# Optimization experiments

Hardware: AMD Instinct MI355X
Metric: run time of the kernel (lower is better)

The kernel has to match this reference:

```python
import jax, jax.numpy as jnp
import numpy as np

TAU = 0.9
TOPK = 8
NUM_LAYERS = 3


def _layer_norm(x, g, b, eps=1e-5):
    mu = jnp.mean(x, axis=-1, keepdims=True)
    var = jnp.var(x, axis=-1, keepdims=True)
    return (x - mu) / jnp.sqrt(var + eps) * g + b


def _forward(x, edge_index, Wi, bi, wp, Wa, ba, ln1_g, ln1_b, ln2_g, ln2_b,
             W1, b1, W2, b2, Wc, bc, Wo, bo):
    N = x.shape[0]
    H = Wi.shape[1]
    # input projection + relu
    x = jax.nn.relu(x @ Wi + bi)
    src, dst = edge_index[0], edge_index[1]
    # ---- priority pi (computed under no_grad, dummy_alpha = 1, x_prev = 0) ----
    delta_x = jnp.sum(jnp.abs(x), axis=1)                      # [N]
    neigh = jax.ops.segment_sum(delta_x[src], dst, num_segments=N)
    pi = jax.lax.stop_gradient(jax.nn.sigmoid(x @ wp + neigh))  # [N]
    # ---- add self loops (selected subgraph == full graph) ----
    loops = jnp.arange(N, dtype=src.dtype)
    src_e = jnp.concatenate([src, loops])
    dst_e = jnp.concatenate([dst, loops])
    Et = src_e.shape[0]
    # ---- edge attention logits: att_mlp(cat[h_i, h_j, p_j]) computed as split matvec ----
    a_dst = x @ Wa[:H]          # contribution of h_i = x[dst]
    a_src = x @ Wa[H:2 * H]     # contribution of h_j = x[src]
    e = a_dst[dst_e] + a_src[src_e] + pi[src_e] * Wa[2 * H] + ba[0]
    e = jax.nn.leaky_relu(e, 0.2) / TAU
    e = jnp.clip(e, -5.0, 5.0)
    exp_e = jnp.exp(e)
    denom = jax.ops.segment_sum(exp_e, dst_e, num_segments=N)
    alpha = exp_e / (denom[dst_e] + 1e-16)
    # ---- per-destination top-k sparsification + renormalization (vectorized) ----
    order = jnp.lexsort((-alpha, dst_e))       # sort by dst, then alpha descending
    dst_s = dst_e[order]
    alpha_s = alpha[order]
    pos = jnp.arange(Et)
    is_new = jnp.concatenate([jnp.ones((1,), bool), dst_s[1:] != dst_s[:-1]])
    grp_start = jax.lax.cummax(jnp.where(is_new, pos, 0))
    rank = pos - grp_start                     # rank within each dst group
    keep = rank < TOPK
    ksum = jax.ops.segment_sum(jnp.where(keep, alpha_s, 0.0), dst_s, num_segments=N)
    alpha_new_s = jnp.where(keep, alpha_s / (ksum[dst_s] + 1e-16), 0.0)
    alpha = jnp.zeros((Et,), x.dtype).at[order].set(alpha_new_s)
    # ---- prenorm blocks with priority-weighted conv (dropout = identity, eval) ----
    h = x
    for l in range(NUM_LAYERS):
        hn = _layer_norm(h, ln1_g[l], ln1_b[l])
        xp = hn @ Wc[l] + bc[l]                               # conv linear
        msg = xp[src_e] * alpha[:, None]                      # [Et, H]
        agg = jax.ops.segment_sum(msg, dst_e, num_segments=N)  # scatter-add
        h = h + jax.nn.relu(agg)
        h2 = _layer_norm(h, ln2_g[l], ln2_b[l])
        h2 = jax.nn.gelu(h2 @ W1[l] + b1[l], approximate=False) @ W2[l] + b2[l]
        h = h + h2
    return h @ Wo + bo


def setup_inputs() -> dict:
    key = jax.random.key(0)
    ks = jax.random.split(key, 10)
    N, E, IN, H, OUT, L, F = 50000, 400000, 256, 256, 64, 3, 512
    def nrm(k, shape, scale):
        return jax.random.normal(k, shape, jnp.float32) * scale
    return {
        "x": nrm(ks[0], (N, IN), 1.0),
        "edge_index": jax.random.randint(ks[1], (2, E), 0, N, dtype=jnp.int32),
        "Wi": nrm(ks[2], (IN, H), IN ** -0.5), "bi": jnp.zeros((H,), jnp.float32),
        "wp": nrm(ks[3], (H,), H ** -0.5),
        "Wa": nrm(ks[4], (2 * H + 1,), (2 * H + 1) ** -0.5), "ba": jnp.zeros((1,), jnp.float32),
        "ln1_g": jnp.ones((L, H), jnp.float32), "ln1_b": jnp.zeros((L, H), jnp.float32),
        "ln2_g": jnp.ones((L, H), jnp.float32), "ln2_b": jnp.zeros((L, H), jnp.float32),
        "W1": nrm(ks[5], (L, H, F), H ** -0.5), "b1": jnp.zeros((L, F), jnp.float32),
        "W2": nrm(ks[6], (L, F, H), F ** -0.5), "b2": jnp.zeros((L, H), jnp.float32),
        "Wc": nrm(ks[7], (L, H, H), H ** -0.5), "bc": jnp.zeros((L, H), jnp.float32),
        "Wo": nrm(ks[8], (H, OUT), H ** -0.5), "bo": jnp.zeros((OUT,), jnp.float32),
    }


def reference(x, edge_index, Wi, bi, wp, Wa, ba, ln1_g, ln1_b, ln2_g, ln2_b,
              W1, b1, W2, b2, Wc, bc, Wo, bo):
    return _forward(x, edge_index, Wi, bi, wp, Wa, ba, ln1_g, ln1_b, ln2_g, ln2_b,
                    W1, b1, W2, b2, Wc, bc, Wo, bo)
```

## Files before the change

### kernel.cpp

```cpp
#include <hip/hip_runtime.h>
#include <math.h>

#define TAUF 0.9f

typedef unsigned int u32;
typedef unsigned short ushort;
typedef __attribute__((ext_vector_type(8))) short short8;
typedef __attribute__((ext_vector_type(8))) _Float16 half8;
typedef __attribute__((ext_vector_type(4))) _Float16 half4;
typedef __attribute__((ext_vector_type(4))) float f32x4;
typedef __attribute__((ext_vector_type(4))) unsigned short us4;

__device__ __forceinline__ ushort f2bf(float f) {
  u32 u = __builtin_bit_cast(u32, f);
  u32 r = (u + 0x7FFFu + ((u >> 16) & 1u)) >> 16;
  return (ushort)r;
}
__device__ __forceinline__ float bf2f(ushort s) {
  u32 u = ((u32)s) << 16;
  return __builtin_bit_cast(float, u);
}

__device__ __forceinline__ float gelu_f(float x) {
  float z = x * 0.70710678118654752f;
  float az = fabsf(z);
  float t = 1.f / fmaf(0.3275911f, az, 1.f);
  float poly = t * fmaf(t, fmaf(t, fmaf(t, fmaf(t, 1.061405429f, -1.453152027f),
                                        1.421413741f), -0.284496736f), 0.254829592f);
  float erfa = fmaf(-poly, __expf(-az * az), 1.f);
  float s = (z < 0.f) ? -erfa : erfa;
  return 0.5f * x * (1.f + s);
}

__device__ __forceinline__ void gload16(const void* g, void* l) {
  __builtin_amdgcn_global_load_lds(
      (const __attribute__((address_space(1))) u32*)g,
      (__attribute__((address_space(3))) u32*)l, 16, 0, 0);
}

__launch_bounds__(256, 2)
__global__ void gemm_in_mfma(const _Float16* __restrict__ Ah, const _Float16* __restrict__ Al,
                             const _Float16* __restrict__ Bh, const _Float16* __restrict__ Bl,
                             const float* __restrict__ bias, const float* __restrict__ Wa,
                             const float* __restrict__ wp, const float* __restrict__ g1,
                             const float* __restrict__ b1g, float* __restrict__ C,
                             ushort* __restrict__ hn, float* __restrict__ delta,
                             float* __restrict__ adst, float* __restrict__ asrc,
                             float* __restrict__ xwp, int M) {
  __shared__ char lds[81920];
  char* As_h = lds;
  char* As_l = lds + 8192;
  char* Bs_h = lds + 16384;
  char* Bs_l = lds + 49152;
  const int tid = threadIdx.x;
  const int wave = tid >> 6, lane = tid & 63;
  const int bm = blockIdx.x * 64;
  const int srow = lane >> 3;
  const int scol = (((lane & 7) ^ srow) << 3);

  f32x4 accH[4][4], accC[4][4];
#pragma unroll
  for (int i = 0; i < 4; ++i)
#pragma unroll
    for (int j = 0; j < 4; ++j) {
      accH[i][j] = (f32x4){0.f, 0.f, 0.f, 0.f};
      accC[i][j] = (f32x4){0.f, 0.f, 0.f, 0.f};
    }

  for (int k0 = 0; k0 < 256; k0 += 64) {
#pragma unroll
    for (int r = 0; r < 2; ++r) {
      const int ch = r * 4 + wave;
      int ar = bm + ch * 8 + srow;
      ar = (ar < M) ? ar : (M - 1);
      gload16(Ah + (size_t)ar * 256 + k0 + scol, As_h + ch * 1024);
      gload16(Al + (size_t)ar * 256 + k0 + scol, As_l + ch * 1024);
    }
#pragma unroll
    for (int r = 0; r < 8; ++r) {
      const int ch = r * 4 + wave;
      const int br = ch * 8 + srow;
      gload16(Bh + (size_t)br * 256 + k0 + scol, Bs_h + ch * 1024);
      gload16(Bl + (size_t)br * 256 + k0 + scol, Bs_l + ch * 1024);
    }
    __syncthreads();
#pragma unroll
    for (int kk = 0; kk < 2; ++kk) {
      const int c = (kk * 32 + (lane >> 4) * 8) * 2;
      half8 ah[4], bh[4];
#pragma unroll
      for (int mi = 0; mi < 4; ++mi) {
        const int rr = mi * 16 + (lane & 15);
        ah[mi] = *(const half8*)(As_h + rr * 128 + (c ^ ((rr & 7) << 4)));
      }
#pragma unroll
      for (int ni = 0; ni < 4; ++ni) {
        const int rr = wave * 64 + ni * 16 + (lane & 15);
        bh[ni] = *(const half8*)(Bs_h + rr * 128 + (c ^ ((rr & 7) << 4)));
      }
#pragma unroll
      for (int mi = 0; mi < 4; ++mi)
#pragma unroll
        for (int ni = 0; ni < 4; ++ni)
          accH[mi][ni] = __builtin_amdgcn_mfma_f32_16x16x32_f16(ah[mi], bh[ni],
                                                                accH[mi][ni], 0, 0, 0);
      half8 al[4];
#pragma unroll
      for (int mi = 0; mi < 4; ++mi) {
        const int rr = mi * 16 + (lane & 15);
        al[mi] = *(const half8*)(As_l + rr * 128 + (c ^ ((rr & 7) << 4)));
      }
#pragma unroll
      for (int mi = 0; mi < 4; ++mi)
#pragma unroll
        for (int ni = 0; ni < 4; ++ni)
          accC[mi][ni] = __builtin_amdgcn_mfma_f32_16x16x32_f16(al[mi], bh[ni],
                                                                accC[mi][ni], 0, 0, 0);
      half8 bl[4];
#pragma unroll
      for (int ni = 0; ni < 4; ++ni) {
        const int rr = wave * 64 + ni * 16 + (lane & 15);
        bl[ni] = *(const half8*)(Bs_l + rr * 128 + (c ^ ((rr & 7) << 4)));
      }
#pragma unroll
      for (int mi = 0; mi < 4; ++mi)
#pragma unroll
        for (int ni = 0; ni < 4; ++ni)
          accC[mi][ni] = __builtin_amdgcn_mfma_f32_16x16x32_f16(ah[mi], bl[ni],
                                                                accC[mi][ni], 0, 0, 0);
    }
    __syncthreads();
  }

  float bb[4], wa0[4], wa1[4], wpv[4], gg[4], gb[4];
#pragma unroll
  for (int ni = 0; ni < 4; ++ni) {
    const int c = wave * 64 + ni * 16 + (lane & 15);
    bb[ni] = bias[c]; wa0[ni] = Wa[c]; wa1[ni] = Wa[256 + c];
    wpv[ni] = wp[c]; gg[ni] = g1[c]; gb[ni] = b1g[c];
  }
  float* red = (float*)lds;
  float* muA = (float*)(lds + 5120);
  float* isA = (float*)(lds + 5376);
  const float inv = 1.f / 2048.f;
#pragma unroll
  for (int mi = 0; mi < 4; ++mi) {
#pragma unroll
    for (int reg = 0; reg < 4; ++reg) {
      const int lrow = mi * 16 + (lane >> 4) * 4 + reg;
      const int row = bm + lrow;
      float v[4];
      float p0 = 0.f, p1 = 0.f, p2 = 0.f, p3 = 0.f, p4 = 0.f;
#pragma unroll
      for (int ni = 0; ni < 4; ++ni) {
        float t = accH[mi][ni][reg] + accC[mi][ni][reg] * inv + bb[ni];
        t = fmaxf(t, 0.f);
        v[ni] = t;
        p0 += t; p1 += t * wa0[ni]; p2 += t * wa1[ni]; p3 += t * wpv[ni];
        p4 += t * t;
      }
      if (row < M) {
#pragma unroll
        for (int ni = 0; ni < 4; ++ni)
          C[(size_t)row * 256 + wave * 64 + ni * 16 + (lane & 15)] = v[ni];
      }
#pragma unroll
      for (int ni = 0; ni < 4; ++ni) accH[mi][ni][reg] = v[ni];
#pragma unroll
      for (int off = 1; off < 16; off <<= 1) {
        p0 += __shfl_xor(p0, off, 64);
        p1 += __shfl_xor(p1, off, 64);
        p2 += __shfl_xor(p2, off, 64);
        p3 += __shfl_xor(p3, off, 64);
        p4 += __shfl_xor(p4, off, 64);
      }
      if ((lane & 15) == 0) {
        red[(0 * 4 + wave) * 64 + lrow] = p0;
        red[(1 * 4 + wave) * 64 + lrow] = p1;
        red[(2 * 4 + wave) * 64 + lrow] = p2;
        red[(3 * 4 + wave) * 64 + lrow] = p3;
        red[(4 * 4 + wave) * 64 + lrow] = p4;
      }
    }
  }
  __syncthreads();
  if (tid < 64) {
    float s0 = 0.f, s1 = 0.f, s2 = 0.f, s3 = 0.f, s4 = 0.f;
#pragma unroll
    for (int w = 0; w < 4; ++w) {
      s0 += red[(0 * 4 + w) * 64 + tid];
      s1 += red[(1 * 4 + w) * 64 + tid];
      s2 += red[(2 * 4 + w) * 64 + tid];
      s3 += red[(3 * 4 + w) * 64 + tid];
      s4 += red[(4 * 4 + w) * 64 + tid];
    }
    const int row = bm + tid;
    if (row < M) {
      delta[row] = s0; adst[row] = s1; asrc[row] = s2; xwp[row] = s3;
    }
    float mu = s0 * (1.f / 256.f);
    muA[tid] = mu;
    isA[tid] = rsqrtf(s4 * (1.f / 256.f) - mu * mu + 1e-5f);
  }
  __syncthreads();
#pragma unroll
  for (int mi = 0; mi < 4; ++mi) {
#pragma unroll
    for (int reg = 0; reg < 4; ++reg) {
      const int lrow = mi * 16 + (lane >> 4) * 4 + reg;
      const int row = bm + lrow;
      if (row >= M) continue;
      const float mu = muA[lrow], is = isA[lrow];
#pragma unroll
      for (int ni = 0; ni < 4; ++ni) {
        const int col = wave * 64 + ni * 16 + (lane & 15);
        hn[(size_t)row * 256 + col] = f2bf((accH[mi][ni][reg] - mu) * is * gg[ni] + gb[ni]);
      }
    }
  }
}

__global__ void xsplit_k(const float* __restrict__ X, _Float16* __restrict__ Xh,
                         _Float16* __restrict__ Xl, int total4) {
  int i = blockIdx.x * 256 + threadIdx.x;
  if (i >= total4) return;
  float4 x = reinterpret_cast<const float4*>(X)[i];
  half4 h, l;
  float xs[4] = {x.x, x.y, x.z, x.w};
#pragma unroll
  for (int j = 0; j < 4; ++j) {
    _Float16 hv = (_Float16)xs[j];
    h[j] = hv;
    l[j] = (_Float16)((xs[j] - (float)hv) * 2048.f);
  }
  reinterpret_cast<half4*>(Xh)[i] = h;
  reinterpret_cast<half4*>(Xl)[i] = l;
}

__global__ void gather_k(const ushort* __restrict__ hn, const int* __restrict__ ksrc,
                         const float* __restrict__ kw, ushort* __restrict__ hagg, int N) {
  int d = blockIdx.x * 4 + (threadIdx.x >> 6);
  if (d >= N) return;
  int lane = threadIdx.x & 63;
  us4 xv[8];
  float w[8];
#pragma unroll
  for (int j = 0; j < 8; ++j) {
    int s = ksrc[(size_t)d * 8 + j];
    w[j] = kw[(size_t)d * 8 + j];
    xv[j] = *reinterpret_cast<const us4*>(hn + (size_t)s * 256 + lane * 4);
  }
  float a0 = 0.f, a1 = 0.f, a2 = 0.f, a3 = 0.f;
#pragma unroll
  for (int j = 0; j < 8; ++j) {
    a0 += w[j] * bf2f(xv[j].x);
    a1 += w[j] * bf2f(xv[j].y);
    a2 += w[j] * bf2f(xv[j].z);
    a3 += w[j] * bf2f(xv[j].w);
  }
  us4 o;
  o.x = f2bf(a0); o.y = f2bf(a1); o.z = f2bf(a2); o.w = f2bf(a3);
  *reinterpret_cast<us4*>(hagg + (size_t)d * 256 + lane * 4) = o;
}

__launch_bounds__(512, 4)
__global__ void gemm_conv_aggln(const ushort* __restrict__ A, const ushort* __restrict__ Bt,
                                const float* __restrict__ bias, const float* __restrict__ g2,
                                const float* __restrict__ b2g, float* __restrict__ h,
                                ushort* __restrict__ hn, int M) {
  __shared__ ushort As[128 * 64];
  __shared__ ushort Bs[256 * 64];
  const int tid = threadIdx.x;
  const int wave = tid >> 6, lane = tid & 63;
  const int bm = blockIdx.x * 128;
  const int wm = (wave >> 2) * 64, wn = (wave & 3) * 64;
  const int srow = lane >> 3;
  const int scol = (((lane & 7) ^ srow) << 3);

  f32x4 acc[4][4];
#pragma unroll
  for (int i = 0; i < 4; ++i)
#pragma unroll
    for (int j = 0; j < 4; ++j) acc[i][j] = (f32x4){0.f, 0.f, 0.f, 0.f};

  for (int k0 = 0; k0 < 256; k0 += 64) {
#pragma unroll
    for (int r = 0; r < 2; ++r) {
      const int ch = r * 8 + wave;
      int ar = bm + ch * 8 + srow;
      ar = (ar < M) ? ar : (M - 1);
      gload16(A + (size_t)ar * 256 + k0 + scol, (char*)As + ch * 1024);
    }
#pragma unroll
    for (int r = 0; r < 4; ++r) {
      const int ch = r * 8 + wave;
      const int br = ch * 8 + srow;
      gload16(Bt + (size_t)br * 256 + k0 + scol, (char*)Bs + ch * 1024);
    }
    __syncthreads();
#pragma unroll
    for (int kk = 0; kk < 2; ++kk) {
      const int c = (kk * 32 + (lane >> 4) * 8) * 2;
      short8 a[4];
#pragma unroll
      for (int mi = 0; mi < 4; ++mi) {
        const int rr = wm + mi * 16 + (lane & 15);
        a[mi] = *(const short8*)((const char*)As + rr * 128 + (c ^ ((rr & 7) << 4)));
      }
#pragma unroll
      for (int ni = 0; ni < 4; ++ni) {
        const int rr = wn + ni * 16 + (lane & 15);
        short8 b = *(const short8*)((const char*)Bs + rr * 128 + (c ^ ((rr & 7) << 4)));
#pragma unroll
        for (int mi = 0; mi < 4; ++mi)
          acc[mi][ni] = __builtin_amdgcn_mfma_f32_16x16x32_bf16(a[mi], b,
                                                                acc[mi][ni], 0, 0, 0);
      }
    }
    __syncthreads();
  }

  float bb[4];
#pragma unroll
  for (int ni = 0; ni < 4; ++ni) bb[ni] = bias[wn + ni * 16 + (lane & 15)];

  float* redS = (float*)As;
  float* redQ = redS + 512;
  float* muA  = redQ + 512;
  float* isA  = muA + 128;

#pragma unroll
  for (int mi = 0; mi < 4; ++mi) {
#pragma unroll
    for (int reg = 0; reg < 4; ++reg) {
      const int lrow = wm + mi * 16 + (lane >> 4) * 4 + reg;
      const int row = bm + lrow;
      const bool ok = (row < M);
      float pS = 0.f, pQ = 0.f;
#pragma unroll
      for (int ni = 0; ni < 4; ++ni) {
        const int col = wn + ni * 16 + (lane & 15);
        float t = fmaxf(acc[mi][ni][reg] + bb[ni], 0.f);
        if (ok) {
          t += h[(size_t)row * 256 + col];
          h[(size_t)row * 256 + col] = t;
        }
        acc[mi][ni][reg] = t;
        pS += t;
        pQ += t * t;
      }
#pragma unroll
      for (int off = 1; off < 16; off <<= 1) {
        pS += __shfl_xor(pS, off, 64);
        pQ += __shfl_xor(pQ, off, 64);
      }
      if ((lane & 15) == 0) {
        redS[(wave & 3) * 128 + lrow] = pS;
        redQ[(wave & 3) * 128 + lrow] = pQ;
      }
    }
  }
  __syncthreads();
  if (tid < 128) {
    float S = redS[tid] + redS[128 + tid] + redS[256 + tid] + redS[384 + tid];
    float Q = redQ[tid] + redQ[128 + tid] + redQ[256 + tid] + redQ[384 + tid];
    float mu = S * (1.f / 256.f);
    muA[tid] = mu;
    isA[tid] = rsqrtf(Q * (1.f / 256.f) - mu * mu + 1e-5f);
  }
  __syncthreads();
  float gg[4], gb[4];
#pragma unroll
  for (int ni = 0; ni < 4; ++ni) {
    gg[ni] = g2[wn + ni * 16 + (lane & 15)];
    gb[ni] = b2g[wn + ni * 16 + (lane & 15)];
  }
#pragma unroll
  for (int mi = 0; mi < 4; ++mi) {
#pragma unroll
    for (int reg = 0; reg < 4; ++reg) {
      const int lrow = wm + mi * 16 + (lane >> 4) * 4 + reg;
      const int row = bm + lrow;
      if (row >= M) continue;
      const float mu = muA[lrow], is = isA[lrow];
#pragma unroll
      for (int ni = 0; ni < 4; ++ni) {
        const int col = wn + ni * 16 + (lane & 15);
        hn[(size_t)row * 256 + col] = f2bf((acc[mi][ni][reg] - mu) * is * gg[ni] + gb[ni]);
      }
    }
  }
}

__launch_bounds__(512, 4)
__global__ void gemm_ffn1(const ushort* __restrict__ A, const ushort* __restrict__ Bt,
                          const float* __restrict__ bias, ushort* __restrict__ u, int M) {
  __shared__ ushort As[128 * 64];
  __shared__ ushort Bs[256 * 64];
  const int tid = threadIdx.x;
  const int wave = tid >> 6, lane = tid & 63;
  const int bm = blockIdx.x * 128;
  const int bn = blockIdx.y * 256;
  const int wm = (wave >> 2) * 64, wn = (wave & 3) * 64;
  const int srow = lane >> 3;
  const int scol = (((lane & 7) ^ srow) << 3);

  f32x4 acc[4][4];
#pragma unroll
  for (int i = 0; i < 4; ++i)
#pragma unroll
    for (int j = 0; j < 4; ++j) acc[i][j] = (f32x4){0.f, 0.f, 0.f, 0.f};

  for (int k0 = 0; k0 < 256; k0 += 64) {
#pragma unroll
    for (int r = 0; r < 2; ++r) {
      const int ch = r * 8 + wave;
      int ar = bm + ch * 8 + srow;
      ar = (ar < M) ? ar : (M - 1);
      gload16(A + (size_t)ar * 256 + k0 + scol, (char*)As + ch * 1024);
    }
#pragma unroll
    for (int r = 0; r < 4; ++r) {
      const int ch = r * 8 + wave;
      const int br = bn + ch * 8 + srow;
      gload16(Bt + (size_t)br * 256 + k0 + scol, (char*)Bs + ch * 1024);
    }
    __syncthreads();
#pragma unroll
    for (int kk = 0; kk < 2; ++kk) {
      const int c = (kk * 32 + (lane >> 4) * 8) * 2;
      short8 a[4];
#pragma unroll
      for (int mi = 0; mi < 4; ++mi) {
        const int rr = wm + mi * 16 + (lane & 15);
        a[mi] = *(const short8*)((const char*)As + rr * 128 + (c ^ ((rr & 7) << 4)));
      }
#pragma unroll
      for (int ni = 0; ni < 4; ++ni) {
        const int rr = wn + ni * 16 + (lane & 15);
        short8 b = *(const short8*)((const char*)Bs + rr * 128 + (c ^ ((rr & 7) << 4)));
#pragma unroll
        for (int mi = 0; mi < 4; ++mi)
          acc[mi][ni] = __builtin_amdgcn_mfma_f32_16x16x32_bf16(a[mi], b,
                                                                acc[mi][ni], 0, 0, 0);
      }
    }
    __syncthreads();
  }

  float bb[4];
#pragma unroll
  for (int ni = 0; ni < 4; ++ni) bb[ni] = bias[bn + wn + ni * 16 + (lane & 15)];
#pragma unroll
  for (int mi = 0; mi < 4; ++mi) {
#pragma unroll
    for (int reg = 0; reg < 4; ++reg) {
      const int row = bm + wm + mi * 16 + (lane >> 4) * 4 + reg;
      if (row >= M) continue;
#pragma unroll
      for (int ni = 0; ni < 4; ++ni) {
        const int col = bn + wn + ni * 16 + (lane & 15);
        u[(size_t)row * 512 + col] = f2bf(gelu_f(acc[mi][ni][reg] + bb[ni]));
      }
    }
  }
}

template <int LAST>
__launch_bounds__(512, 4)
__global__ void gemm_ffn2ln(const ushort* __restrict__ A, const ushort* __restrict__ Bt,
                            const float* __restrict__ bias, const float* __restrict__ g1,
                            const float* __restrict__ b1g, float* __restrict__ h,
                            ushort* __restrict__ hn, int M) {
  __shared__ ushort As[128 * 64];
  __shared__ ushort Bs[256 * 64];
  const int tid = threadIdx.x;
  const int wave = tid >> 6, lane = tid & 63;
  const int bm = blockIdx.x * 128;
  const int wm = (wave >> 2) * 64, wn = (wave & 3) * 64;
  const int srow = lane >> 3;
  const int scol = (((lane & 7) ^ srow) << 3);

  f32x4 acc[4][4];
#pragma unroll
  for (int i = 0; i < 4; ++i)
#pragma unroll
    for (int j = 0; j < 4; ++j) acc[i][j] = (f32x4){0.f, 0.f, 0.f, 0.f};

  for (int k0 = 0; k0 < 512; k0 += 64) {
#pragma unroll
    for (int r = 0; r < 2; ++r) {
      const int ch = r * 8 + wave;
      int ar = bm + ch * 8 + srow;
      ar = (ar < M) ? ar : (M - 1);
      gload16(A + (size_t)ar * 512 + k0 + scol, (char*)As + ch * 1024);
    }
#pragma unroll
    for (int r = 0; r < 4; ++r) {
      const int ch = r * 8 + wave;
      const int br = ch * 8 + srow;
      gload16(Bt + (size_t)br * 512 + k0 + scol, (char*)Bs + ch * 1024);
    }
    __syncthreads();
#pragma unroll
    for (int kk = 0; kk < 2; ++kk) {
      const int c = (kk * 32 + (lane >> 4) * 8) * 2;
      short8 a[4];
#pragma unroll
      for (int mi = 0; mi < 4; ++mi) {
        const int rr = wm + mi * 16 + (lane & 15);
        a[mi] = *(const short8*)((const char*)As + rr * 128 + (c ^ ((rr & 7) << 4)));
      }
#pragma unroll
      for (int ni = 0; ni < 4; ++ni) {
        const int rr = wn + ni * 16 + (lane & 15);
        short8 b = *(const short8*)((const char*)Bs + rr * 128 + (c ^ ((rr & 7) << 4)));
#pragma unroll
        for (int mi = 0; mi < 4; ++mi)
          acc[mi][ni] = __builtin_amdgcn_mfma_f32_16x16x32_bf16(a[mi], b,
                                                                acc[mi][ni], 0, 0, 0);
      }
    }
    __syncthreads();
  }

  float bb[4];
#pragma unroll
  for (int ni = 0; ni < 4; ++ni) bb[ni] = bias[wn + ni * 16 + (lane & 15)];

  float* redS = (float*)As;
  float* redQ = redS + 512;
  float* muA  = redQ + 512;
  float* isA  = muA + 128;

#pragma unroll
  for (int mi = 0; mi < 4; ++mi) {
#pragma unroll
    for (int reg = 0; reg < 4; ++reg) {
      const int lrow = wm + mi * 16 + (lane >> 4) * 4 + reg;
      const int row = bm + lrow;
      const bool ok = (row < M);
      float pS = 0.f, pQ = 0.f;
#pragma unroll
      for (int ni = 0; ni < 4; ++ni) {
        const int col = wn + ni * 16 + (lane & 15);
        float t = acc[mi][ni][reg] + bb[ni];
        if (ok) t += h[(size_t)row * 256 + col];
        acc[mi][ni][reg] = t;
        if (LAST) {
          if (ok) hn[(size_t)row * 256 + col] = f2bf(t);
        } else {
          if (ok) h[(size_t)row * 256 + col] = t;
          pS += t;
          pQ += t * t;
        }
      }
      if (!LAST) {
#pragma unroll
        for (int off = 1; off < 16; off <<= 1) {
          pS += __shfl_xor(pS, off, 64);
          pQ += __shfl_xor(pQ, off, 64);
        }
        if ((lane & 15) == 0) {
          redS[(wave & 3) * 128 + lrow] = pS;
          redQ[(wave & 3) * 128 + lrow] = pQ;
        }
      }
    }
  }
  if (LAST) return;
  __syncthreads();
  if (tid < 128) {
    float S = redS[tid] + redS[128 + tid] + redS[256 + tid] + redS[384 + tid];
    float Q = redQ[tid] + redQ[128 + tid] + redQ[256 + tid] + redQ[384 + tid];
    float mu = S * (1.f / 256.f);
    muA[tid] = mu;
    isA[tid] = rsqrtf(Q * (1.f / 256.f) - mu * mu + 1e-5f);
  }
  __syncthreads();
  float gg[4], gb[4];
#pragma unroll
  for (int ni = 0; ni < 4; ++ni) {
    gg[ni] = g1[wn + ni * 16 + (lane & 15)];
    gb[ni] = b1g[wn + ni * 16 + (lane & 15)];
  }
#pragma unroll
  for (int mi = 0; mi < 4; ++mi) {
#pragma unroll
    for (int reg = 0; reg < 4; ++reg) {
      const int lrow = wm + mi * 16 + (lane >> 4) * 4 + reg;
      const int row = bm + lrow;
      if (row >= M) continue;
      const float mu = muA[lrow], is = isA[lrow];
#pragma unroll
      for (int ni = 0; ni < 4; ++ni) {
        const int col = wn + ni * 16 + (lane & 15);
        hn[(size_t)row * 256 + col] = f2bf((acc[mi][ni][reg] - mu) * is * gg[ni] + gb[ni]);
      }
    }
  }
}

__launch_bounds__(256)
__global__ void gemm_out(const ushort* __restrict__ A, const ushort* __restrict__ Bt,
                         const float* __restrict__ bias, float* __restrict__ C, int M) {
  __shared__ ushort As[128 * 64];
  __shared__ ushort Bs[64 * 64];
  const int tid = threadIdx.x;
  const int wave = tid >> 6, lane = tid & 63;
  const int bm = blockIdx.x * 128;
  const int wm = wave * 32;
  const int srow = lane >> 3;
  const int scol = (((lane & 7) ^ srow) << 3);
  f32x4 acc[2][4];
#pragma unroll
  for (int i = 0; i < 2; ++i)
#pragma unroll
    for (int j = 0; j < 4; ++j) acc[i][j] = (f32x4){0.f, 0.f, 0.f, 0.f};

  for (int k0 = 0; k0 < 256; k0 += 64) {
#pragma unroll
    for (int r = 0; r < 4; ++r) {
      const int ch = r * 4 + wave;
      int ar = bm + ch * 8 + srow;
      ar = (ar < M) ? ar : (M - 1);
      gload16(A + (size_t)ar * 256 + k0 + scol, (char*)As + ch * 1024);
    }
#pragma unroll
    for (int r = 0; r < 2; ++r) {
      const int ch = r * 4 + wave;
      const int br = ch * 8 + srow;
      gload16(Bt + (size_t)br * 256 + k0 + scol, (char*)Bs + ch * 1024);
    }
    __syncthreads();
#pragma unroll
    for (int kk = 0; kk < 2; ++kk) {
      const int c = (kk * 32 + (lane >> 4) * 8) * 2;
      short8 a[2], b[4];
#pragma unroll
      for (int mi = 0; mi < 2; ++mi) {
        const int rr = wm + mi * 16 + (lane & 15);
        a[mi] = *(const short8*)((const char*)As + rr * 128 + (c ^ ((rr & 7) << 4)));
      }
#pragma unroll
      for (int ni = 0; ni < 4; ++ni) {
        const int rr = ni * 16 + (lane & 15);
        b[ni] = *(const short8*)((const char*)Bs + rr * 128 + (c ^ ((rr & 7) << 4)));
      }
#pragma unroll
      for (int mi = 0; mi < 2; ++mi)
#pragma unroll
        for (int ni = 0; ni < 4; ++ni)
          acc[mi][ni] = __builtin_amdgcn_mfma_f32_16x16x32_bf16(a[mi], b[ni],
                                                                acc[mi][ni], 0, 0, 0);
    }
    __syncthreads();
  }
  float bb[4];
#pragma unroll
  for (int ni = 0; ni < 4; ++ni) bb[ni] = bias[ni * 16 + (lane & 15)];
#pragma unroll
  for (int mi = 0; mi < 2; ++mi) {
#pragma unroll
    for (int reg = 0; reg < 4; ++reg) {
      const int row = bm + wm + mi * 16 + (lane >> 4) * 4 + reg;
      if (row >= M) continue;
#pragma unroll
      for (int ni = 0; ni < 4; ++ni) {
        const int col = ni * 16 + (lane & 15);
        C[(size_t)row * 64 + col] = acc[mi][ni][reg] + bb[ni];
      }
    }
  }
}

#define W_IN 65536
#define W_TOTAL (196608 + 393216 + 393216 + 16384)
__global__ void prep_k(const float* __restrict__ Wi, const float* __restrict__ Wc,
                       const float* __restrict__ W1, const float* __restrict__ W2,
                       const float* __restrict__ Wo, _Float16* __restrict__ WiTh,
                       _Float16* __restrict__ WiTl, ushort* __restrict__ WcT,
                       ushort* __restrict__ W1T, ushort* __restrict__ W2T,
                       ushort* __restrict__ WoT, float* __restrict__ zbase, int zn) {
  int i = blockIdx.x * 256 + threadIdx.x;
  if (i < W_IN) {
    int n = i >> 8, k = i & 255;
    float w = Wi[(size_t)k * 256 + n];
    _Float16 hv = (_Float16)w;
    WiTh[i] = hv;
    WiTl[i] = (_Float16)((w - (float)hv) * 2048.f);
  } else if ((i -= W_IN) < W_TOTAL) {
    int j = i;
    if (j < 196608) {
      int l = j / 65536, r = j % 65536, n = r >> 8, k = r & 255;
      WcT[j] = f2bf(Wc[(size_t)l * 65536 + k * 256 + n]);
    } else if ((j -= 196608) < 393216) {
      int l = j / 131072, r = j % 131072, n = r >> 8, k = r & 255;
      W1T[j] = f2bf(W1[(size_t)l * 131072 + k * 512 + n]);
    } else if ((j -= 393216) < 393216) {
      int l = j / 131072, r = j % 131072, n = r >> 9, k = r & 511;
      W2T[j] = f2bf(W2[(size_t)l * 131072 + k * 256 + n]);
    } else {
      j -= 393216;
      int n = j >> 8, k = j & 255;
      WoT[j] = f2bf(Wo[k * 64 + n]);
    }
  } else {
    int z = i - W_TOTAL;
    if (z < zn) zbase[z] = 0.f;
  }
}

__global__ void neigh_k(const int* __restrict__ src, const int* __restrict__ dst,
                        const float* __restrict__ delta, float* __restrict__ neigh, int E) {
  int e = blockIdx.x * 256 + threadIdx.x;
  if (e < E) atomicAdd(&neigh[dst[e]], delta[src[e]]);
}

__global__ void logits_k(const int* __restrict__ src, const int* __restrict__ dst,
                         const float* __restrict__ adst, const float* __restrict__ asrc,
                         const float* __restrict__ xwp, const float* __restrict__ neigh,
                         const float* __restrict__ Wa, const float* __restrict__ ba,
                         float* __restrict__ expe, float* __restrict__ denom,
                         int* __restrict__ cnt, int* __restrict__ slots,
                         int E, int Et, int N) {
  int e = blockIdx.x * 256 + threadIdx.x;
  if (e >= Et) return;
  int s, d;
  if (e < E) { s = src[e]; d = dst[e]; } else { s = e - E; d = s; }
  float pis = 1.f / (1.f + expf(-(xwp[s] + neigh[s])));
  float v = adst[d] + asrc[s] + pis * Wa[512] + ba[0];
  v = (v >= 0.f ? v : 0.2f * v) / TAUF;
  v = fminf(fmaxf(v, -5.f), 5.f);
  float ex = expf(v);
  expe[e] = ex;
  atomicAdd(&denom[d], ex);
  int p = atomicAdd(&cnt[d], 1);
  if (p < 64) slots[(size_t)p * N + d] = e;
}

__device__ __forceinline__ bool better(float a, int e, float a2, int e2) {
  return a > a2 || (a == a2 && e < e2);
}

__global__ void topk_k(const int* __restrict__ cnt, const int* __restrict__ slots,
                       const float* __restrict__ expe, const float* __restrict__ denom,
                       const int* __restrict__ src, int* __restrict__ ksrc,
                       float* __restrict__ kw, int N, int E) {
  int d = blockIdx.x * 256 + threadIdx.x;
  if (d >= N) return;
  int deg = min(cnt[d], 64);
  float D = denom[d] + 1e-16f;
  float av[8]; int ai[8]; int kc = 0;
  for (int t = 0; t < deg; ++t) {
    int e = slots[(size_t)t * N + d];
    float a = expe[e] / D;
    if (kc < 8) {
      int p = kc++;
      while (p > 0 && better(a, e, av[p - 1], ai[p - 1])) {
        av[p] = av[p - 1]; ai[p] = ai[p - 1]; --p;
      }
      av[p] = a; ai[p] = e;
    } else if (better(a, e, av[7], ai[7])) {
      int p = 7;
      while (p > 0 && better(a, e, av[p - 1], ai[p - 1])) {
        av[p] = av[p - 1]; ai[p] = ai[p - 1]; --p;
      }
      av[p] = a; ai[p] = e;
    }
  }
  float ks = 0.f;
  for (int j = 0; j < kc; ++j) ks += av[j];
  float inv = 1.f / (ks + 1e-16f);
#pragma unroll
  for (int j = 0; j < 8; ++j) {
    if (j < kc) {
      int e = ai[j];
      ksrc[(size_t)d * 8 + j] = (e < E) ? src[e] : (e - E);
      kw[(size_t)d * 8 + j] = av[j] * inv;
    } else {
      ksrc[(size_t)d * 8 + j] = 0;
      kw[(size_t)d * 8 + j] = 0.f;
    }
  }
}

extern "C" void kernel_launch(void* const* d_in, const int* in_sizes, int n_in,
                              void* d_out, int out_size, void* d_ws, size_t ws_size,
                              hipStream_t stream) {
  const float* X   = (const float*)d_in[0];
  const int*   EI  = (const int*)d_in[1];
  const float* Wi  = (const float*)d_in[2];
  const float* bi  = (const float*)d_in[3];
  const float* wp  = (const float*)d_in[4];
  const float* Wa  = (const float*)d_in[5];
  const float* ba  = (const float*)d_in[6];
  const float* l1g = (const float*)d_in[7];
  const float* l1b = (const float*)d_in[8];
  const float* l2g = (const float*)d_in[9];
  const float* l2b = (const float*)d_in[10];
  const float* W1  = (const float*)d_in[11];
  const float* b1  = (const float*)d_in[12];
  const float* W2  = (const float*)d_in[13];
  const float* b2  = (const float*)d_in[14];
  const float* Wc  = (const float*)d_in[15];
  const float* bc  = (const float*)d_in[16];
  const float* Wo  = (const float*)d_in[17];
  const float* bo  = (const float*)d_in[18];

  const int N = in_sizes[0] / 256;
  const int E = in_sizes[1] / 2;
  const int Et = E + N;
  const int* srcp = EI;
  const int* dstp = EI + E;

  float* ws = (float*)d_ws;
  size_t off = 0;
  auto alloc = [&](size_t n) { float* p = ws + off; off += n; return p; };
  const size_t NH = (size_t)N * 256;
  float*  h    = alloc(NH);
  ushort* hn   = (ushort*)alloc(NH / 2);
  ushort* hagg = (ushort*)alloc(NH / 2);
  float*  ualias = alloc(NH);
  ushort* u    = (ushort*)ualias;
  _Float16* Xh = (_Float16*)ualias;
  _Float16* Xl = Xh + NH;
  _Float16* WiTh = (_Float16*)alloc(65536 / 2);
  _Float16* WiTl = (_Float16*)alloc(65536 / 2);
  ushort* WcT  = (ushort*)alloc(3 * 65536 / 2);
  ushort* W1T  = (ushort*)alloc(3 * 131072 / 2);
  ushort* W2T  = (ushort*)alloc(3 * 131072 / 2);
  ushort* WoT  = (ushort*)alloc(16384 / 2);
  float* delta = alloc(N);
  float* adst  = alloc(N);
  float* asrc  = alloc(N);
  float* xwp   = alloc(N);
  float* expe  = alloc(Et);
  float* neigh = alloc(N);
  float* denom = alloc(N);
  int*   cnt   = (int*)alloc(N);
  int*   slots = (int*)alloc((size_t)N * 64);
  int*   ksrc  = (int*)alloc((size_t)N * 8);
  float* kw    = alloc((size_t)N * 8);

  prep_k<<<(W_IN + W_TOTAL + 3 * N + 255) / 256, 256, 0, stream>>>(
      Wi, Wc, W1, W2, Wo, WiTh, WiTl, WcT, W1T, W2T, WoT, neigh, 3 * N);
  xsplit_k<<<((int)(NH / 4) + 255) / 256, 256, 0, stream>>>(X, Xh, Xl, (int)(NH / 4));

  gemm_in_mfma<<<(N + 63) / 64, 256, 0, stream>>>(
      Xh, Xl, WiTh, WiTl, bi, Wa, wp, l1g, l1b, h, hn,
      delta, adst, asrc, xwp, N);
  neigh_k<<<(E + 255) / 256, 256, 0, stream>>>(srcp, dstp, delta, neigh, E);
  logits_k<<<(Et + 255) / 256, 256, 0, stream>>>(srcp, dstp, adst, asrc, xwp, neigh,
                                                 Wa, ba, expe, denom, cnt, slots,
                                                 E, Et, N);
  topk_k<<<(N + 255) / 256, 256, 0, stream>>>(cnt, slots, expe, denom, srcp,
                                              ksrc, kw, N, E);

  const int GM = (N + 127) / 128;
  for (int l = 0; l < 3; ++l) {
    gather_k<<<(N + 3) / 4, 256, 0, stream>>>(hn, ksrc, kw, hagg, N);
    gemm_conv_aggln<<<GM, 512, 0, stream>>>(
        hagg, WcT + (size_t)l * 65536, bc + l * 256,
        l2g + l * 256, l2b + l * 256, h, hn, N);
    gemm_ffn1<<<dim3(GM, 2), 512, 0, stream>>>(
        hn, W1T + (size_t)l * 131072, b1 + l * 512, u, N);
    if (l < 2)
      gemm_ffn2ln<0><<<GM, 512, 0, stream>>>(
          u, W2T + (size_t)l * 131072, b2 + l * 256,
          l1g + (l + 1) * 256, l1b + (l + 1) * 256, h, hn, N);
    else
      gemm_ffn2ln<1><<<GM, 512, 0, stream>>>(
          u, W2T + (size_t)l * 131072, b2 + l * 256,
          nullptr, nullptr, h, hn, N);
  }
  gemm_out<<<(N + 127) / 128, 256, 0, stream>>>(hn, WoT, bo, (float*)d_out, N);
}
```

Measured before the change: 646.3 us.

## Fuse fp32-to-fp16 hi/lo input split into input projection GEMM

Removes the separate xsplit kernel. The input GEMM now reads fp32 X directly and converts it to fp16 high/low parts in registers before storing them to LDS. This avoids writing and re-reading the split arrays through global memory. The K tile shrinks from 64 to 32, halving LDS to 40KB and raising launch bounds to 4 blocks per SM, at the cost of twice as many K iterations and barriers with no async loads for A.

```diff
diff --git a/kernel.cpp b/kernel.cpp
--- a/kernel.cpp
+++ b/kernel.cpp
@@ -7,7 +7,6 @@
 typedef unsigned short ushort;
 typedef __attribute__((ext_vector_type(8))) short short8;
 typedef __attribute__((ext_vector_type(8))) _Float16 half8;
-typedef __attribute__((ext_vector_type(4))) _Float16 half4;
 typedef __attribute__((ext_vector_type(4))) float f32x4;
 typedef __attribute__((ext_vector_type(4))) unsigned short us4;
 
@@ -38,8 +37,8 @@
       (__attribute__((address_space(3))) u32*)l, 16, 0, 0);
 }
 
-__launch_bounds__(256, 2)
-__global__ void gemm_in_mfma(const _Float16* __restrict__ Ah, const _Float16* __restrict__ Al,
+__launch_bounds__(256, 4)
+__global__ void gemm_in_mfma(const float* __restrict__ X,
                              const _Float16* __restrict__ Bh, const _Float16* __restrict__ Bl,
                              const float* __restrict__ bias, const float* __restrict__ Wa,
                              const float* __restrict__ wp, const float* __restrict__ g1,
@@ -47,16 +46,20 @@
                              ushort* __restrict__ hn, float* __restrict__ delta,
                              float* __restrict__ adst, float* __restrict__ asrc,
                              float* __restrict__ xwp, int M) {
-  __shared__ char lds[81920];
+  __shared__ char lds[40960];
   char* As_h = lds;
-  char* As_l = lds + 8192;
-  char* Bs_h = lds + 16384;
-  char* Bs_l = lds + 49152;
+  char* As_l = lds + 4096;
+  char* Bs_h = lds + 8192;
+  char* Bs_l = lds + 24576;
   const int tid = threadIdx.x;
   const int wave = tid >> 6, lane = tid & 63;
   const int bm = blockIdx.x * 64;
-  const int srow = lane >> 3;
-  const int scol = (((lane & 7) ^ srow) << 3);
+
+  const int arow = tid >> 2;
+  const int achunk = tid & 3;
+  const int abyte = arow * 64 + ((achunk ^ (arow & 3)) << 4);
+  const int brow = lane >> 2;
+  const int bcol = (((lane & 3) ^ (brow & 3)) << 3);
 
   f32x4 accH[4][4], accC[4][4];
 #pragma unroll
@@ -67,68 +70,73 @@
       accC[i][j] = (f32x4){0.f, 0.f, 0.f, 0.f};
     }
 
-  for (int k0 = 0; k0 < 256; k0 += 64) {
-#pragma unroll
-    for (int r = 0; r < 2; ++r) {
+  int ar = bm + arow;
+  ar = (ar < M) ? ar : (M - 1);
+  const float* xrow = X + (size_t)ar * 256 + achunk * 8;
+
+  for (int k0 = 0; k0 < 256; k0 += 32) {
+    float4 x0 = *reinterpret_cast<const float4*>(xrow + k0);
+    float4 x1 = *reinterpret_cast<const float4*>(xrow + k0 + 4);
+    float xs[8] = {x0.x, x0.y, x0.z, x0.w, x1.x, x1.y, x1.z, x1.w};
+    half8 hh, ll;
+#pragma unroll
+    for (int j = 0; j < 8; ++j) {
+      _Float16 hv = (_Float16)xs[j];
+      hh[j] = hv;
+      ll[j] = (_Float16)((xs[j] - (float)hv) * 2048.f);
+    }
+    *reinterpret_cast<half8*>(As_h + abyte) = hh;
+    *reinterpret_cast<half8*>(As_l + abyte) = ll;
+#pragma unroll
+    for (int r = 0; r < 4; ++r) {
       const int ch = r * 4 + wave;
-      int ar = bm + ch * 8 + srow;
-      ar = (ar < M) ? ar : (M - 1);
-      gload16(Ah + (size_t)ar * 256 + k0 + scol, As_h + ch * 1024);
-      gload16(Al + (size_t)ar * 256 + k0 + scol, As_l + ch * 1024);
-    }
-#pragma unroll
-    for (int r = 0; r < 8; ++r) {
-      const int ch = r * 4 + wave;
-      const int br = ch * 8 + srow;
-      gload16(Bh + (size_t)br * 256 + k0 + scol, Bs_h + ch * 1024);
-      gload16(Bl + (size_t)br * 256 + k0 + scol, Bs_l + ch * 1024);
-    }
-    __syncthreads();
-#pragma unroll
-    for (int kk = 0; kk < 2; ++kk) {
-      const int c = (kk * 32 + (lane >> 4) * 8) * 2;
-      half8 ah[4], bh[4];
-#pragma unroll
-      for (int mi = 0; mi < 4; ++mi) {
-        const int rr = mi * 16 + (lane & 15);
-        ah[mi] = *(const half8*)(As_h + rr * 128 + (c ^ ((rr & 7) << 4)));
-      }
-#pragma unroll
-      for (int ni = 0; ni < 4; ++ni) {
-        const int rr = wave * 64 + ni * 16 + (lane & 15);
-        bh[ni] = *(const half8*)(Bs_h + rr * 128 + (c ^ ((rr & 7) << 4)));
-      }
-#pragma unroll
-      for (int mi = 0; mi < 4; ++mi)
-#pragma unroll
-        for (int ni = 0; ni < 4; ++ni)
-          accH[mi][ni] = __builtin_amdgcn_mfma_f32_16x16x32_f16(ah[mi], bh[ni],
-                                                                accH[mi][ni], 0, 0, 0);
-      half8 al[4];
-#pragma unroll
-      for (int mi = 0; mi < 4; ++mi) {
-        const int rr = mi * 16 + (lane & 15);
-        al[mi] = *(const half8*)(As_l + rr * 128 + (c ^ ((rr & 7) << 4)));
-      }
-#pragma unroll
-      for (int mi = 0; mi < 4; ++mi)
-#pragma unroll
-        for (int ni = 0; ni < 4; ++ni)
-          accC[mi][ni] = __builtin_amdgcn_mfma_f32_16x16x32_f16(al[mi], bh[ni],
-                                                                accC[mi][ni], 0, 0, 0);
-      half8 bl[4];
-#pragma unroll
-      for (int ni = 0; ni < 4; ++ni) {
-        const int rr = wave * 64 + ni * 16 + (lane & 15);
-        bl[ni] = *(const half8*)(Bs_l + rr * 128 + (c ^ ((rr & 7) << 4)));
-      }
-#pragma unroll
-      for (int mi = 0; mi < 4; ++mi)
-#pragma unroll
-        for (int ni = 0; ni < 4; ++ni)
-          accC[mi][ni] = __builtin_amdgcn_mfma_f32_16x16x32_f16(ah[mi], bl[ni],
-                                                                accC[mi][ni], 0, 0, 0);
-    }
+      const int br = ch * 16 + brow;
+      gload16(Bh + (size_t)br * 256 + k0 + bcol, Bs_h + ch * 1024);
+      gload16(Bl + (size_t)br * 256 + k0 + bcol, Bs_l + ch * 1024);
+    }
+    __syncthreads();
+    const int fs = lane >> 4;
+    half8 ah[4], bh[4];
+#pragma unroll
+    for (int mi = 0; mi < 4; ++mi) {
+      const int rr = mi * 16 + (lane & 15);
+      ah[mi] = *(const half8*)(As_h + rr * 64 + ((fs ^ (rr & 3)) << 4));
+    }
+#pragma unroll
+    for (int ni = 0; ni < 4; ++ni) {
+      const int rr = wave * 64 + ni * 16 + (lane & 15);
+      bh[ni] = *(const half8*)(Bs_h + rr * 64 + ((fs ^ (rr & 3)) << 4));
+    }
+#pragma unroll
+    for (int mi = 0; mi < 4; ++mi)
+#pragma unroll
+      for (int ni = 0; ni < 4; ++ni)
+        accH[mi][ni] = __builtin_amdgcn_mfma_f32_16x16x32_f16(ah[mi], bh[ni],
+                                                              accH[mi][ni], 0, 0, 0);
+    half8 al[4];
+#pragma unroll
+    for (int mi = 0; mi < 4; ++mi) {
+      const int rr = mi * 16 + (lane & 15);
+      al[mi] = *(const half8*)(As_l + rr * 64 + ((fs ^ (rr & 3)) << 4));
+    }
+#pragma unroll
+    for (int mi = 0; mi < 4; ++mi)
+#pragma unroll
+      for (int ni = 0; ni < 4; ++ni)
+        accC[mi][ni] = __builtin_amdgcn_mfma_f32_16x16x32_f16(al[mi], bh[ni],
+                                                              accC[mi][ni], 0, 0, 0);
+    half8 bl[4];
+#pragma unroll
+    for (int ni = 0; ni < 4; ++ni) {
+      const int rr = wave * 64 + ni * 16 + (lane & 15);
+      bl[ni] = *(const half8*)(Bs_l + rr * 64 + ((fs ^ (rr & 3)) << 4));
+    }
+#pragma unroll
+    for (int mi = 0; mi < 4; ++mi)
+#pragma unroll
+      for (int ni = 0; ni < 4; ++ni)
+        accC[mi][ni] = __builtin_amdgcn_mfma_f32_16x16x32_f16(ah[mi], bl[ni],
+                                                              accC[mi][ni], 0, 0, 0);
     __syncthreads();
   }
 
@@ -218,23 +226,6 @@
       }
     }
   }
-}
-
-__global__ void xsplit_k(const float* __restrict__ X, _Float16* __restrict__ Xh,
-                         _Float16* __restrict__ Xl, int total4) {
-  int i = blockIdx.x * 256 + threadIdx.x;
-  if (i >= total4) return;
-  float4 x = reinterpret_cast<const float4*>(X)[i];
-  half4 h, l;
-  float xs[4] = {x.x, x.y, x.z, x.w};
-#pragma unroll
-  for (int j = 0; j < 4; ++j) {
-    _Float16 hv = (_Float16)xs[j];
-    h[j] = hv;
-    l[j] = (_Float16)((xs[j] - (float)hv) * 2048.f);
-  }
-  reinterpret_cast<half4*>(Xh)[i] = h;
-  reinterpret_cast<half4*>(Xl)[i] = l;
 }
 
 __global__ void gather_k(const ushort* __restrict__ hn, const int* __restrict__ ksrc,
@@ -821,10 +812,7 @@
   float*  h    = alloc(NH);
   ushort* hn   = (ushort*)alloc(NH / 2);
   ushort* hagg = (ushort*)alloc(NH / 2);
-  float*  ualias = alloc(NH);
-  ushort* u    = (ushort*)ualias;
-  _Float16* Xh = (_Float16*)ualias;
-  _Float16* Xl = Xh + NH;
+  ushort* u    = (ushort*)alloc(NH);
   _Float16* WiTh = (_Float16*)alloc(65536 / 2);
   _Float16* WiTl = (_Float16*)alloc(65536 / 2);
   ushort* WcT  = (ushort*)alloc(3 * 65536 / 2);
@@ -845,10 +833,9 @@
 
   prep_k<<<(W_IN + W_TOTAL + 3 * N + 255) / 256, 256, 0, stream>>>(
       Wi, Wc, W1, W2, Wo, WiTh, WiTl, WcT, W1T, W2T, WoT, neigh, 3 * N);
-  xsplit_k<<<((int)(NH / 4) + 255) / 256, 256, 0, stream>>>(X, Xh, Xl, (int)(NH / 4));
 
   gemm_in_mfma<<<(N + 63) / 64, 256, 0, stream>>>(
-      Xh, Xl, WiTh, WiTl, bi, Wa, wp, l1g, l1b, h, hn,
+      X, WiTh, WiTl, bi, Wa, wp, l1g, l1b, h, hn,
       delta, adst, asrc, xwp, N);
   neigh_k<<<(E + 255) / 256, 256, 0, stream>>>(srcp, dstp, delta, neigh, E);
   logits_k<<<(Et + 255) / 256, 256, 0, stream>>>(srcp, dstp, adst, asrc, xwp, neigh,
```

Result: slower. 876.4 us (+35.6%).
